# Optimization experiments

Hardware: AMD Instinct MI355X
Metric: run time of the kernel (lower is better)

Reference implementation:

```python
import jax, jax.numpy as jnp
import numpy as np

WINDOW_SIZE = 2
MAX_POW = 3


def setup_inputs() -> dict:
    # Pure integer grid dims; no tensors needed for this index-generation module.
    return {"t": 8, "h": 32, "w": 32}


def reference(t, h, w):
    N = t * h * w
    L = N + 2
    # patch_coords: [N, 3] grid coordinates (ij indexing)
    gt, gh, gw = jnp.meshgrid(jnp.arange(t), jnp.arange(h), jnp.arange(w), indexing="ij")
    patch_coords = jnp.stack([gt, gh, gw], axis=-1).reshape(N, 3).astype(jnp.int32)
    all_coords = jnp.concatenate(
        [
            jnp.array([[-1, -1, -1]], dtype=jnp.int32),
            patch_coords,
            jnp.array([[t, h, w]], dtype=jnp.int32),
        ],
        axis=0,
    )  # [L, 3]

    # Per-dimension absolute diffs, each [L, N] (avoids materializing [L, N, 3])
    diffs = [
        jnp.abs(patch_coords[None, :, d] - all_coords[:, None, d]) for d in range(3)
    ]

    # Local window mask: all three |diff| <= window_size
    local_mask = (
        (diffs[0] <= WINDOW_SIZE) & (diffs[1] <= WINDOW_SIZE) & (diffs[2] <= WINDOW_SIZE)
    )

    # Strided sparse mask: |diff_d| == 2**p along exactly one axis, 0 along the others
    sparse_mask = jnp.zeros((L, N), dtype=bool)
    for p in range(MAX_POW):
        off = 2 ** p
        for d in range(3):
            m = diffs[d] == off
            m = m & (diffs[(d + 1) % 3] == 0) & (diffs[(d + 2) % 3] == 0)
            sparse_mask = sparse_mask | m
    mask = local_mask | sparse_mask  # [L, N]

    # Sampled patch index j (0-based) maps to value j+1; sentinels 0 and L-1 always kept.
    # Extended mask over value space [0, L): column j selected <=> value j in row's index set.
    ones_col = jnp.ones((L, 1), dtype=bool)
    ext = jnp.concatenate([ones_col, mask, ones_col], axis=1)  # [L, L]
    counts = ext.sum(axis=1)  # per-row number of indices (>= 2)
    K = int(jnp.max(counts))  # concrete pad width (data-dependent; computed eagerly)

    # Stable argsort of ~ext packs selected column indices (== values, sorted ascending)
    # to the front of each row, matching torch.unique's sorted output.
    order = jnp.argsort(~ext, axis=1, stable=True)[:, :K]
    valid_mask = jnp.arange(K)[None, :] < counts[:, None]  # [L, K]
    idx_tensor = jnp.where(valid_mask, order, 0).astype(jnp.int32)
    return idx_tensor, valid_mask, all_coords
```

## Files before the change

kernel.cpp:

```cpp
#include <hip/hip_runtime.h>


__global__ __launch_bounds__(256) void hybrid_sparse_idx_wave(
        const int* __restrict__ pt, const int* __restrict__ ph,
        const int* __restrict__ pw, int* __restrict__ out, int out_size) {
    const int t = pt[0], h = ph[0], w = pw[0];
    const int hw = h * w;
    const int N = t * hw;
    const int L = N + 2;
    const int K = (out_size / L - 3) / 2;

    int* __restrict__ out_idx   = out;
    int* __restrict__ out_valid = out + (size_t)L * K;
    int* __restrict__ out_crd   = out + (size_t)2 * L * K;

    const int lane    = threadIdx.x & 63;
    const int wave    = threadIdx.x >> 6;
    const int wperblk = blockDim.x >> 6;
    const unsigned long long lanemask_lt = (1ull << lane) - 1ull;

    for (int i = blockIdx.x * wperblk + wave; i < L;
         i += gridDim.x * wperblk) {
        int at, ah, aw;
        if (i == 0)          { at = -1; ah = -1; aw = -1; }
        else if (i == L - 1) { at = t;  ah = h;  aw = w;  }
        else {
            int j = i - 1;
            at = j / hw;
            int r = j - at * hw;
            ah = r / w;
            aw = r - ah * w;
        }
        if (lane < 3) {
            int v = (lane == 0) ? at : ((lane == 1) ? ah : aw);
            out_crd[3 * i + lane] = v;
        }

        int* ridx = out_idx   + (size_t)i * K;
        int* rval = out_valid + (size_t)i * K;

        if (lane == 0) { ridx[0] = 0; rval[0] = 1; }
        int pos = 1;

        for (int base = 0; base < 729; base += 64) {
            const int c = base + lane;
            bool keep = false;
            int  j    = 0;
            if (c < 729) {
                const int ot = c / 81;
                const int rc = c - ot * 81;
                const int oh = rc / 9;
                const int ow = rc - oh * 9;
                const int jt = at - 4 + ot;
                const int jh = ah - 4 + oh;
                const int jw = aw - 4 + ow;
                if (jt >= 0 && jt < t && jh >= 0 && jh < h &&
                    jw >= 0 && jw < w) {
                    const int adt = ot >= 4 ? ot - 4 : 4 - ot;
                    const int adh = oh >= 4 ? oh - 4 : 4 - oh;
                    const int adw = ow >= 4 ? ow - 4 : 4 - ow;
                    const bool local  = (adt <= 2) & (adh <= 2) & (adw <= 2);
                    const bool sparse =
                        ((adt == 4) & (adh == 0) & (adw == 0)) |
                        ((adh == 4) & (adt == 0) & (adw == 0)) |
                        ((adw == 4) & (adt == 0) & (adh == 0));
                    keep = local | sparse;
                    j = (jt * h + jh) * w + jw;
                }
            }
            const unsigned long long ball = __ballot(keep);
            if (keep) {
                const int p = pos + __popcll(ball & lanemask_lt);
                if (p < K) { ridx[p] = j + 1; rval[p] = 1; }
            }
            pos += __popcll(ball);
        }

        if (lane == 0 && pos < K) { ridx[pos] = L - 1; rval[pos] = 1; }
        ++pos;

        for (int k = pos + lane; k < K; k += 64) { ridx[k] = 0; rval[k] = 0; }
    }
}

extern "C" void kernel_launch(void* const* d_in, const int* in_sizes, int n_in,
                              void* d_out, int out_size, void* d_ws, size_t ws_size,
                              hipStream_t stream) {
    (void)in_sizes; (void)n_in; (void)d_ws; (void)ws_size;
    const int* pt = (const int*)d_in[0];
    const int* ph = (const int*)d_in[1];
    const int* pw = (const int*)d_in[2];
    int* out = (int*)d_out;

    const int block = 256;
    const int rows_per_block = block / 64;
    const int grid = 2049;
    hybrid_sparse_idx_wave<<<grid, block, 0, stream>>>(pt, ph, pw, out,
                                                       out_size);
    (void)rows_per_block;
}
```

Measured before the change: 69.70 us.

## Stage rows in LDS and write outputs with vectorized stores using a compile-time mask

The keep pattern over the 9x9x9 offset cube is now computed at compile time as twelve 64-bit masks, so the per-lane window and sparse tests collapse to a bit lookup plus a bounds check. Each wave packs its row of indices into a small LDS buffer and then writes both the index row and the valid row with int4 stores. Before, each selected element was scattered to global memory with separate index and valid writes, plus a padding loop. Rows of length K that are not a multiple of four give unaligned int4 global stores, and the code assumes the row count never exceeds the 136-entry LDS slot.

Result: faster. 65.53 us (-6.0%).

```diff
diff --git a/kernel.cpp b/kernel.cpp
--- a/kernel.cpp
+++ b/kernel.cpp
@@ -1,85 +1,120 @@
 #include <hip/hip_runtime.h>
 
 
-__global__ __launch_bounds__(256) void hybrid_sparse_idx_wave(
+struct Masks {
+    unsigned long long keep[12];
+};
+
+constexpr Masks make_masks() {
+    Masks m{};
+    for (int i = 0; i < 12; ++i) m.keep[i] = 0ull;
+    for (int c = 0; c < 729; ++c) {
+        const int ot = c / 81;
+        const int oh = (c % 81) / 9;
+        const int ow = c % 9;
+        const int adt = ot >= 4 ? ot - 4 : 4 - ot;
+        const int adh = oh >= 4 ? oh - 4 : 4 - oh;
+        const int adw = ow >= 4 ? ow - 4 : 4 - ow;
+        const bool local = (adt <= 2) && (adh <= 2) && (adw <= 2);
+        const bool sparse =
+            ((adt == 4) && (adh == 0) && (adw == 0)) ||
+            ((adh == 4) && (adt == 0) && (adw == 0)) ||
+            ((adw == 4) && (adt == 0) && (adh == 0));
+        if (local || sparse) m.keep[c >> 6] |= (1ull << (c & 63));
+    }
+    return m;
+}
+
+__global__ __launch_bounds__(256) void hybrid_sparse_idx_lds(
         const int* __restrict__ pt, const int* __restrict__ ph,
         const int* __restrict__ pw, int* __restrict__ out, int out_size) {
+    constexpr Masks M = make_masks();
+    __shared__ int slds[4][136];
+
     const int t = pt[0], h = ph[0], w = pw[0];
     const int hw = h * w;
     const int N = t * hw;
     const int L = N + 2;
     const int K = (out_size / L - 3) / 2;
 
-    int* __restrict__ out_idx   = out;
-    int* __restrict__ out_valid = out + (size_t)L * K;
-    int* __restrict__ out_crd   = out + (size_t)2 * L * K;
+    int* __restrict__ out_idx = out;
+    int* __restrict__ out_val = out + (size_t)L * K;
+    int* __restrict__ out_crd = out + (size_t)2 * L * K;
 
-    const int lane    = threadIdx.x & 63;
-    const int wave    = threadIdx.x >> 6;
-    const int wperblk = blockDim.x >> 6;
-    const unsigned long long lanemask_lt = (1ull << lane) - 1ull;
+    const int lane = threadIdx.x & 63;
+    const int wv   = threadIdx.x >> 6;
+    const unsigned long long lt = (1ull << lane) - 1ull;
+    int* __restrict__ my = slds[wv];
 
-    for (int i = blockIdx.x * wperblk + wave; i < L;
-         i += gridDim.x * wperblk) {
+    for (int i = blockIdx.x * 4 + wv; i < L; i += gridDim.x * 4) {
         int at, ah, aw;
         if (i == 0)          { at = -1; ah = -1; aw = -1; }
         else if (i == L - 1) { at = t;  ah = h;  aw = w;  }
         else {
-            int j = i - 1;
+            const int j = i - 1;
             at = j / hw;
-            int r = j - at * hw;
+            const int r = j - at * hw;
             ah = r / w;
             aw = r - ah * w;
         }
-        if (lane < 3) {
-            int v = (lane == 0) ? at : ((lane == 1) ? ah : aw);
-            out_crd[3 * i + lane] = v;
-        }
+        if (lane < 3)
+            out_crd[3 * i + lane] = (lane == 0) ? at : ((lane == 1) ? ah : aw);
 
-        int* ridx = out_idx   + (size_t)i * K;
-        int* rval = out_valid + (size_t)i * K;
-
-        if (lane == 0) { ridx[0] = 0; rval[0] = 1; }
+        if (lane == 0) my[0] = 0;
         int pos = 1;
 
-        for (int base = 0; base < 729; base += 64) {
-            const int c = base + lane;
-            bool keep = false;
-            int  j    = 0;
-            if (c < 729) {
-                const int ot = c / 81;
-                const int rc = c - ot * 81;
-                const int oh = rc / 9;
-                const int ow = rc - oh * 9;
-                const int jt = at - 4 + ot;
-                const int jh = ah - 4 + oh;
-                const int jw = aw - 4 + ow;
-                if (jt >= 0 && jt < t && jh >= 0 && jh < h &&
-                    jw >= 0 && jw < w) {
-                    const int adt = ot >= 4 ? ot - 4 : 4 - ot;
-                    const int adh = oh >= 4 ? oh - 4 : 4 - oh;
-                    const int adw = ow >= 4 ? ow - 4 : 4 - ow;
-                    const bool local  = (adt <= 2) & (adh <= 2) & (adw <= 2);
-                    const bool sparse =
-                        ((adt == 4) & (adh == 0) & (adw == 0)) |
-                        ((adh == 4) & (adt == 0) & (adw == 0)) |
-                        ((adw == 4) & (adt == 0) & (adh == 0));
-                    keep = local | sparse;
-                    j = (jt * h + jh) * w + jw;
-                }
-            }
-            const unsigned long long ball = __ballot(keep);
-            if (keep) {
-                const int p = pos + __popcll(ball & lanemask_lt);
-                if (p < K) { ridx[p] = j + 1; rval[p] = 1; }
-            }
+#pragma unroll
+        for (int chunk = 0; chunk < 12; ++chunk) {
+            const unsigned c = chunk * 64u + (unsigned)lane;
+            const bool pat = (M.keep[chunk] >> lane) & 1ull;
+            const unsigned ot = c / 81u;
+            const unsigned rc = c - ot * 81u;
+            const unsigned oh = rc / 9u;
+            const unsigned ow = rc - oh * 9u;
+            const int jt = at - 4 + (int)ot;
+            const int jh = ah - 4 + (int)oh;
+            const int jw = aw - 4 + (int)ow;
+            const bool inb = ((unsigned)jt < (unsigned)t) &
+                             ((unsigned)jh < (unsigned)h) &
+                             ((unsigned)jw < (unsigned)w);
+            const bool keepv = pat & inb;
+            const unsigned long long ball = __ballot(keepv);
+            if (keepv)
+                my[pos + __popcll(ball & lt)] = (jt * h + jh) * w + jw + 1;
             pos += __popcll(ball);
         }
 
-        if (lane == 0 && pos < K) { ridx[pos] = L - 1; rval[pos] = 1; }
-        ++pos;
+        if (lane == 0) my[pos] = L - 1;
+        const int cnt = pos + 1;
 
-        for (int k = pos + lane; k < K; k += 64) { ridx[k] = 0; rval[k] = 0; }
+        const int K4 = (K + 3) & ~3;
+        for (int k = cnt + lane; k < K4; k += 64) my[k] = 0;
+
+        asm volatile("s_waitcnt lgkmcnt(0)" ::: "memory");
+
+        const int nvec = K >> 2;
+        const int rem  = K & 3;
+        if (lane < nvec) {
+            const int b = lane << 2;
+            const int4 v = *reinterpret_cast<const int4*>(&my[b]);
+            *reinterpret_cast<int4*>(&out_idx[(size_t)i * K + b]) = v;
+        }
+        if (lane < rem)
+            out_idx[(size_t)i * K + (nvec << 2) + lane] = my[(nvec << 2) + lane];
+
+        if (lane < nvec) {
+            const int b = lane << 2;
+            int4 v;
+            v.x = (b + 0) < cnt;
+            v.y = (b + 1) < cnt;
+            v.z = (b + 2) < cnt;
+            v.w = (b + 3) < cnt;
+            *reinterpret_cast<int4*>(&out_val[(size_t)i * K + b]) = v;
+        }
+        if (lane < rem) {
+            const int k = (nvec << 2) + lane;
+            out_val[(size_t)i * K + k] = (k < cnt) ? 1 : 0;
+        }
     }
 }
 
@@ -93,9 +128,6 @@
     int* out = (int*)d_out;
 
     const int block = 256;
-    const int rows_per_block = block / 64;
-    const int grid = 2049;
-    hybrid_sparse_idx_wave<<<grid, block, 0, stream>>>(pt, ph, pw, out,
-                                                       out_size);
-    (void)rows_per_block;
+    const int grid  = 2049;
+    hybrid_sparse_idx_lds<<<grid, block, 0, stream>>>(pt, ph, pw, out, out_size);
 }
```
